# Performance work log

Measured on AMD Instinct MI355X. Metric: run time of the kernel, lower is better.

## Reference

```python
import jax, jax.numpy as jnp
import numpy as np

EPS_COS = 1e-8   # torch cosine_similarity eps
EPS_DEN = 1e-6   # denominator eps in original loss
TEMP = 0.1


def setup_inputs() -> dict:
    key = jax.random.key(0)
    k1, _ = jax.random.split(key)
    N, D = 16384, 2048
    x = jax.random.normal(k1, (N, D), dtype=jnp.float32)
    pos_pair = jnp.arange(2, dtype=jnp.int64)  # (i, j) = (0, 1), i != j
    return {"x": x, "pos_pair": pos_pair}


def reference(x, pos_pair):
    # x: [N, D]; pos_pair: [2] int indices (i, j)
    i = pos_pair[0]
    j = pos_pair[1]
    xi = x[i]                                        # [D] anchor
    # cosine similarity of anchor against every row (single fused matvec)
    dots = x @ xi                                    # [N]
    norms = jnp.maximum(jnp.linalg.norm(x, axis=1), EPS_COS)   # [N]
    ni = jnp.maximum(jnp.linalg.norm(xi), EPS_COS)
    cos = dots / (norms * ni)                        # [N]
    e = jnp.exp(cos / TEMP)                          # [N]
    # denominator sums over all k != i (k == j included, as in original)
    mask = jnp.arange(x.shape[0]) != i
    denominator = jnp.sum(jnp.where(mask, e, 0.0))
    nominator = e[j]
    loss = -jnp.log(nominator / (denominator + EPS_DEN))
    return loss.reshape(1)  # original returns shape [1]
```

## Files before the change

### kernel.cpp

```cpp
#include <hip/hip_runtime.h>
#include <math.h>

#define D 2048
#define EPS_COS 1e-8f
#define EPS_DEN 1e-6f
#define INV_TEMP 10.0f
#define TPB 256
#define WPB 4
#define NBLK 4096

__device__ __forceinline__ void get_ij(const int* __restrict__ p, int n,
                                       int& i, int& j) {
    int i32 = p[0], j32 = p[1];
    if (i32 >= 0 && i32 < n && j32 >= 0 && j32 < n && i32 != j32) {
        i = i32; j = j32; return;
    }
    const long long* p64 = (const long long*)p;
    i = (int)p64[0]; j = (int)p64[1];
}

__global__ __launch_bounds__(TPB)
void e_kernel(const float* __restrict__ x, const int* __restrict__ pos,
              float* __restrict__ part, float* __restrict__ nom, int n) {
    int i, j;
    get_ij(pos, n, i, j);
    const int lane = threadIdx.x & 63;
    const int wave = threadIdx.x >> 6;
    const int row  = blockIdx.x * WPB + wave;

    const float4* __restrict__ xr = (const float4*)(x + (size_t)row * D);
    const float4* __restrict__ xi = (const float4*)(x + (size_t)i * D);

    float4 a[8], b[8];
#pragma unroll
    for (int w = 0; w < 8; ++w) a[w] = xr[lane + w * 64];
#pragma unroll
    for (int w = 0; w < 8; ++w) b[w] = xi[lane + w * 64];

    float dot = 0.f, sq = 0.f, sqi = 0.f;
#pragma unroll
    for (int w = 0; w < 8; ++w) {
        dot = fmaf(a[w].x, b[w].x, fmaf(a[w].y, b[w].y,
              fmaf(a[w].z, b[w].z, fmaf(a[w].w, b[w].w, dot))));
        sq  = fmaf(a[w].x, a[w].x, fmaf(a[w].y, a[w].y,
              fmaf(a[w].z, a[w].z, fmaf(a[w].w, a[w].w, sq))));
        sqi = fmaf(b[w].x, b[w].x, fmaf(b[w].y, b[w].y,
              fmaf(b[w].z, b[w].z, fmaf(b[w].w, b[w].w, sqi))));
    }
#pragma unroll
    for (int off = 32; off; off >>= 1) {
        dot += __shfl_down(dot, off);
        sq  += __shfl_down(sq,  off);
        sqi += __shfl_down(sqi, off);
    }

    __shared__ float s_den[WPB];
    if (lane == 0) {
        float nk = fmaxf(sqrtf(sq),  EPS_COS);
        float ni = fmaxf(sqrtf(sqi), EPS_COS);
        float e  = expf(INV_TEMP * dot / (nk * ni));
        s_den[wave] = (row != i) ? e : 0.f;
        if (row == j) *nom = e;
    }
    __syncthreads();
    if (threadIdx.x == 0)
        part[blockIdx.x] = (s_den[0] + s_den[1]) + (s_den[2] + s_den[3]);
}

__global__ __launch_bounds__(1024)
void loss_kernel(const float* __restrict__ part, const float* __restrict__ nom,
                 float* __restrict__ out) {
    const int t = threadIdx.x;
    const float4 v = ((const float4*)part)[t];
    float s = (v.x + v.y) + (v.z + v.w);
#pragma unroll
    for (int off = 32; off; off >>= 1) s += __shfl_down(s, off);

    __shared__ float ls[16];
    if ((t & 63) == 0) ls[t >> 6] = s;
    __syncthreads();

    if (t == 0) {
        float den = 0.f;
#pragma unroll
        for (int w = 0; w < 16; ++w) den += ls[w];
        out[0] = -logf(nom[0] / (den + EPS_DEN));
    }
}

extern "C" void kernel_launch(void* const* d_in, const int* in_sizes, int n_in,
                              void* d_out, int out_size, void* d_ws, size_t ws_size,
                              hipStream_t stream) {
    const float* x    = (const float*)d_in[0];
    const int*   pos  = (const int*)d_in[1];
    float*       out  = (float*)d_out;
    float*       part = (float*)d_ws;
    float*       nom  = (float*)d_ws + NBLK;

    const int n = in_sizes[0] / D;

    e_kernel<<<NBLK, TPB, 0, stream>>>(x, pos, part, nom, n);
    loss_kernel<<<1, 1024, 0, stream>>>(part, nom, out);
}
```

Baseline: 188.4 us.

## Process four rows per wave with double-buffered loads and reuse anchor norm

Each wave now handles four consecutive rows instead of one. It loads the anchor row and computes its norm once, then prefetches the next row into a second register buffer while reducing the current one. The aim is to cut redundant anchor reloads and anchor-norm reductions and to overlap memory loads with compute. In exchange the grid drops to 1024 blocks and register use rises, which may lower the number of waves in flight for this bandwidth-bound read of 128MB. The final reduction kernel is resized to match the smaller partial count.

```diff
diff --git a/kernel.cpp b/kernel.cpp
--- a/kernel.cpp
+++ b/kernel.cpp
@@ -7,7 +7,7 @@
 #define INV_TEMP 10.0f
 #define TPB 256
 #define WPB 4
-#define NBLK 4096
+#define RPW 4
 
 __device__ __forceinline__ void get_ij(const int* __restrict__ p, int n,
                                        int& i, int& j) {
@@ -24,66 +24,89 @@
               float* __restrict__ part, float* __restrict__ nom, int n) {
     int i, j;
     get_ij(pos, n, i, j);
-    const int lane = threadIdx.x & 63;
-    const int wave = threadIdx.x >> 6;
-    const int row  = blockIdx.x * WPB + wave;
+    const int lane  = threadIdx.x & 63;
+    const int wave  = threadIdx.x >> 6;
+    const int gwave = blockIdx.x * WPB + wave;
+    const int row0  = gwave * RPW;
 
-    const float4* __restrict__ xr = (const float4*)(x + (size_t)row * D);
     const float4* __restrict__ xi = (const float4*)(x + (size_t)i * D);
 
-    float4 a[8], b[8];
+    float4 b[8], a[2][8];
+    const float4* __restrict__ p0 = (const float4*)(x + (size_t)row0 * D);
 #pragma unroll
-    for (int w = 0; w < 8; ++w) a[w] = xr[lane + w * 64];
+    for (int w = 0; w < 8; ++w) a[0][w] = p0[lane + w * 64];
 #pragma unroll
     for (int w = 0; w < 8; ++w) b[w] = xi[lane + w * 64];
 
-    float dot = 0.f, sq = 0.f, sqi = 0.f;
+    float sqi = 0.f;
 #pragma unroll
-    for (int w = 0; w < 8; ++w) {
-        dot = fmaf(a[w].x, b[w].x, fmaf(a[w].y, b[w].y,
-              fmaf(a[w].z, b[w].z, fmaf(a[w].w, b[w].w, dot))));
-        sq  = fmaf(a[w].x, a[w].x, fmaf(a[w].y, a[w].y,
-              fmaf(a[w].z, a[w].z, fmaf(a[w].w, a[w].w, sq))));
+    for (int w = 0; w < 8; ++w)
         sqi = fmaf(b[w].x, b[w].x, fmaf(b[w].y, b[w].y,
               fmaf(b[w].z, b[w].z, fmaf(b[w].w, b[w].w, sqi))));
-    }
 #pragma unroll
-    for (int off = 32; off; off >>= 1) {
-        dot += __shfl_down(dot, off);
-        sq  += __shfl_down(sq,  off);
-        sqi += __shfl_down(sqi, off);
+    for (int off = 32; off; off >>= 1) sqi += __shfl_down(sqi, off);
+    const float ni = fmaxf(sqrtf(sqi), EPS_COS);
+
+    float den_local = 0.f, ej = 0.f;
+
+#pragma unroll
+    for (int r = 0; r < RPW; ++r) {
+        if (r + 1 < RPW) {
+            const float4* __restrict__ pn =
+                (const float4*)(x + (size_t)(row0 + r + 1) * D);
+#pragma unroll
+            for (int w = 0; w < 8; ++w) a[(r + 1) & 1][w] = pn[lane + w * 64];
+        }
+        float dot = 0.f, sq = 0.f;
+#pragma unroll
+        for (int w = 0; w < 8; ++w) {
+            float4 c = a[r & 1][w];
+            dot = fmaf(c.x, b[w].x, fmaf(c.y, b[w].y,
+                  fmaf(c.z, b[w].z, fmaf(c.w, b[w].w, dot))));
+            sq  = fmaf(c.x, c.x, fmaf(c.y, c.y,
+                  fmaf(c.z, c.z, fmaf(c.w, c.w, sq))));
+        }
+#pragma unroll
+        for (int off = 32; off; off >>= 1) {
+            dot += __shfl_down(dot, off);
+            sq  += __shfl_down(sq,  off);
+        }
+        if (lane == 0) {
+            const int row = row0 + r;
+            float e = expf(INV_TEMP * dot / (fmaxf(sqrtf(sq), EPS_COS) * ni));
+            if (row != i) den_local += e;
+            if (row == j) ej = e;
+        }
     }
 
     __shared__ float s_den[WPB];
     if (lane == 0) {
-        float nk = fmaxf(sqrtf(sq),  EPS_COS);
-        float ni = fmaxf(sqrtf(sqi), EPS_COS);
-        float e  = expf(INV_TEMP * dot / (nk * ni));
-        s_den[wave] = (row != i) ? e : 0.f;
-        if (row == j) *nom = e;
+        s_den[wave] = den_local;
+        if (ej != 0.f) *nom = ej;
     }
     __syncthreads();
     if (threadIdx.x == 0)
         part[blockIdx.x] = (s_den[0] + s_den[1]) + (s_den[2] + s_den[3]);
 }
 
-__global__ __launch_bounds__(1024)
+__global__ __launch_bounds__(256)
 void loss_kernel(const float* __restrict__ part, const float* __restrict__ nom,
-                 float* __restrict__ out) {
+                 float* __restrict__ out, int nblk) {
     const int t = threadIdx.x;
-    const float4 v = ((const float4*)part)[t];
-    float s = (v.x + v.y) + (v.z + v.w);
+    float s = 0.f;
+    if (t < nblk / 4) {
+        float4 v = ((const float4*)part)[t];
+        s = (v.x + v.y) + (v.z + v.w);
+    }
 #pragma unroll
     for (int off = 32; off; off >>= 1) s += __shfl_down(s, off);
 
-    __shared__ float ls[16];
+    __shared__ float ls[4];
     if ((t & 63) == 0) ls[t >> 6] = s;
     __syncthreads();
 
     if (t == 0) {
-        float den = 0.f;
-#pragma unroll
-        for (int w = 0; w < 16; ++w) den += ls[w];
+        float den = (ls[0] + ls[1]) + (ls[2] + ls[3]);
         out[0] = -logf(nom[0] / (den + EPS_DEN));
     }
 }
@@ -94,11 +117,13 @@
     const float* x    = (const float*)d_in[0];
     const int*   pos  = (const int*)d_in[1];
     float*       out  = (float*)d_out;
-    float*       part = (float*)d_ws;
-    float*       nom  = (float*)d_ws + NBLK;
 
-    const int n = in_sizes[0] / D;
+    const int n    = in_sizes[0] / D;
+    const int nblk = n / (WPB * RPW);
 
-    e_kernel<<<NBLK, TPB, 0, stream>>>(x, pos, part, nom, n);
-    loss_kernel<<<1, 1024, 0, stream>>>(part, nom, out);
+    float* part = (float*)d_ws;
+    float* nom  = (float*)d_ws + nblk;
+
+    e_kernel<<<nblk, TPB, 0, stream>>>(x, pos, part, nom, n);
+    loss_kernel<<<1, 256, 0, stream>>>(part, nom, out, nblk);
 }
```

After: 189.9 us. About the same (+0.8%).
